# Kernel optimization log

Hardware: AMD Instinct MI355X
Metric: run time of the kernel (lower is better)

## Reference

```python
import jax, jax.numpy as jnp
import numpy as np

LAYER = 2
B, L, N, N2, S, M, D = 128, 50, 12, 12, 20, 12, 100


def _l2norm(x, eps=1e-12):
    # torch F.normalize: x / max(||x||_2, eps) over last dim
    n = jnp.sqrt(jnp.sum(x * x, axis=-1, keepdims=True))
    return x / jnp.maximum(n, eps)


def setup_inputs() -> dict:
    key = jax.random.key(0)
    ks = jax.random.split(key, 10)
    return {
        "sess_self": jax.random.normal(ks[0], (B, L, D), jnp.float32),
        "sess_neighbor": jax.random.normal(ks[1], (B, L, N, D), jnp.float32),
        "sess_neighbor2": jax.random.normal(ks[2], (B, L, N, N2, D), jnp.float32),
        "tar_self": jax.random.normal(ks[3], (B, S, D), jnp.float32),
        "tar_neighbor": jax.random.normal(ks[4], (B, S, M, D), jnp.float32),
        "w1": jax.random.normal(ks[5], (LAYER, D, D), jnp.float32) * 0.1,
        "w2": jax.random.normal(ks[6], (LAYER, D, 1), jnp.float32) * 0.1,
        "w3": jax.random.normal(ks[7], (LAYER, 2 * D, D), jnp.float32) * 0.1,
        "w4": jax.random.normal(ks[8], (LAYER, D, 1), jnp.float32) * 0.1,
        "session_len": jax.random.randint(ks[9], (B,), 1, 50).astype(jnp.int64),
    }


def _forward(sess_self, sess_neighbor, sess_neighbor2, tar_self, tar_neighbor, w1, w2, w3, w4):
    b, s = sess_self.shape[0], tar_self.shape[1]
    l, d = sess_self.shape[1], sess_self.shape[2]
    # sess_embedding_layer: list of [B,S,L,D]; target: list of [B,S,D]
    sess_layers = [jnp.broadcast_to(sess_self[:, None, :, :], (b, s, l, d))]
    tar_layers = [tar_self]
    sn = sess_neighbor  # may be updated by 2-hop aggregation
    for i in range(LAYER):
        # --- session neighbor attention: mul -> linear -> leaky_relu -> linear -> softmax(N) -> sum ---
        mean_sess = jnp.mean(sess_layers[i], axis=1)                     # [B,L,D]
        att = (mean_sess[:, :, None, :] * sn) @ w1[i]                    # [B,L,N,D]
        att = jax.nn.leaky_relu(att, negative_slope=0.2)
        att = jax.nn.softmax(att @ w2[i], axis=-2)                       # [B,L,N,1]
        total = jnp.sum(att * sn, axis=-2)                               # [B,L,D]
        emb = _l2norm(total)
        sess_layers.append(jnp.broadcast_to(emb[:, None, :, :], (b, s, l, d)))
        # --- 2-hop neighbor aggregation (only first layer when layer>1) ---
        if i <= 0 and LAYER > 1:
            att2 = (sn[:, :, :, None, :] * sess_neighbor2) @ w1[i]       # [B,L,N,N2,D]
            att2 = jax.nn.leaky_relu(att2, negative_slope=0.2)
            att2 = jax.nn.softmax(att2 @ w2[i], axis=-2)                 # [B,L,N,N2,1]
            sn = jnp.sum(att2 * sess_neighbor2, axis=-2)                 # [B,L,N,D]
        # --- target neighbor attention ---
        sess_last = sess_layers[i - 1][:, :, :1, :]                      # [B,S,1,D]
        t = tar_layers[i]                                                # [B,S,D]
        cat = jnp.concatenate(
            [t[:, :, None, :] * tar_neighbor, sess_last + tar_neighbor], axis=-1)  # [B,S,M,2D]
        a = jnp.tanh(cat @ w3[i])                                        # [B,S,M,D]
        a = jax.nn.softmax(a @ w4[i], axis=-2)                           # [B,S,M,1]
        tot = jnp.sum(a * tar_neighbor, axis=-2)                         # [B,S,D]
        ti = _l2norm((tot + tar_layers[0]) * 0.5)
        tar_layers.append(ti)
        tar_layers = tar_layers + tar_layers  # faithful: list doubles each layer
    return jnp.stack(sess_layers, axis=0), jnp.stack(tar_layers, axis=0)


def reference(sess_self, sess_neighbor, sess_neighbor2, tar_self, tar_neighbor, w1, w2, w3, w4, session_len):
    return _forward(sess_self, sess_neighbor, sess_neighbor2, tar_self, tar_neighbor, w1, w2, w3, w4)
```

## Files before the change

### kernel.cpp

```cpp
#include <hip/hip_runtime.h>
#include <cmath>

#define CB 128
#define CL 50
#define CN 12
#define CS 20
#define CM 12
#define CD 100

typedef __attribute__((ext_vector_type(8))) short short8;
typedef __attribute__((ext_vector_type(4))) float f32x4;

__device__ __forceinline__ unsigned short f2bf(float f) {
    unsigned int u = __float_as_uint(f);
    u += 0x7FFFu + ((u >> 16) & 1u);
    return (unsigned short)(u >> 16);
}
__device__ __forceinline__ float4 mul4(float4 a, float4 b) {
    return make_float4(a.x * b.x, a.y * b.y, a.z * b.z, a.w * b.w);
}
__device__ __forceinline__ float4 add4(float4 a, float4 b) {
    return make_float4(a.x + b.x, a.y + b.y, a.z + b.z, a.w + b.w);
}
__device__ __forceinline__ short8 pack8(float4 a, float4 b) {
    short8 v;
    v[0] = (short)f2bf(a.x); v[1] = (short)f2bf(a.y);
    v[2] = (short)f2bf(a.z); v[3] = (short)f2bf(a.w);
    v[4] = (short)f2bf(b.x); v[5] = (short)f2bf(b.y);
    v[6] = (short)f2bf(b.z); v[7] = (short)f2bf(b.w);
    return v;
}

__global__ void prep_weights_kernel(const float* __restrict__ w1,
                                    const float* __restrict__ w3,
                                    unsigned short* __restrict__ w1t,
                                    unsigned short* __restrict__ w3t)
{
    int idx = blockIdx.x * 256 + threadIdx.x;
    const int TOT1 = 2 * 112 * 128;
    const int TOT3 = 2 * 112 * 224;
    if (idx < TOT1) {
        int l = idx / (112 * 128);
        int r = idx - l * (112 * 128);
        int n = r / 128, k = r - (r / 128) * 128;
        float v = (n < CD && k < CD) ? w1[l * CD * CD + k * CD + n] : 0.f;
        w1t[idx] = f2bf(v);
    } else if (idx < TOT1 + TOT3) {
        int j = idx - TOT1;
        int l = j / (112 * 224);
        int r = j - l * (112 * 224);
        int n = r / 224, k = r - (r / 224) * 224;
        float v = (n < CD && k < 2 * CD) ? w3[l * 2 * CD * CD + k * CD + n] : 0.f;
        w3t[j] = f2bf(v);
    }
}

__global__ __launch_bounds__(256) void neigh_mfma_kernel(
    const float* __restrict__ a0, const float* __restrict__ c0,
    float* __restrict__ o0, int nb0, int l20,
    const float* __restrict__ a1, const float* __restrict__ c1,
    float* __restrict__ o1, int l21,
    const unsigned short* __restrict__ w1t,
    const float* __restrict__ w2)
{
    __shared__ __align__(16) unsigned short sB[112 * 128];

    const int tid = threadIdx.x;
    const int wave = tid >> 6, lane = tid & 63;
    const int lhi = lane >> 4, llo = lane & 15;

    const float *ap, *cp; float* op; int l2f, g0;
    if ((int)blockIdx.x < nb0) {
        ap = a0; cp = c0; op = o0; l2f = l20; g0 = blockIdx.x * 8;
    } else {
        ap = a1; cp = c1; op = o1; l2f = l21; g0 = (blockIdx.x - nb0) * 8;
    }

    for (int i = tid; i < 1792; i += 256) {
        int n = i >> 4, kc = i & 15;
        short8 v = *(const short8*)(w1t + n * 128 + kc * 8);
        char* dst = (char*)sB + n * 256 + ((kc ^ (n & 7)) << 4);
        *(short8*)dst = v;
    }

    short8 af[2][4];
#pragma unroll
    for (int mt = 0; mt < 2; ++mt) {
        const int g = g0 + wave * 2 + mt;
        const int n = (llo < CN) ? llo : 0;
        const float* cpr = cp + ((size_t)g * CN + n) * CD;
        const float* apr = ap + (size_t)g * CD;
#pragma unroll
        for (int ks = 0; ks < 4; ++ks) {
            const int k0 = ks * 32 + lhi * 8;
            if (ks < 3) {
                float4 cv0 = *(const float4*)(cpr + k0);
                float4 cv1 = *(const float4*)(cpr + k0 + 4);
                float4 av0 = *(const float4*)(apr + k0);
                float4 av1 = *(const float4*)(apr + k0 + 4);
                af[mt][ks] = pack8(mul4(av0, cv0), mul4(av1, cv1));
            } else if (lhi == 0) {
                float4 cv0 = *(const float4*)(cpr + 96);
                float4 av0 = *(const float4*)(apr + 96);
                float4 z = make_float4(0.f, 0.f, 0.f, 0.f);
                af[mt][ks] = pack8(mul4(av0, cv0), z);
            } else {
                af[mt][ks] = (short8){0, 0, 0, 0, 0, 0, 0, 0};
            }
        }
    }
    __syncthreads();

    f32x4 acc[2][7];
#pragma unroll
    for (int mt = 0; mt < 2; ++mt)
#pragma unroll
        for (int nt = 0; nt < 7; ++nt) acc[mt][nt] = (f32x4){0.f, 0.f, 0.f, 0.f};

    const char* pB = (const char*)sB;
    const int bxor = llo & 7;
#pragma unroll
    for (int ks = 0; ks < 4; ++ks) {
        const int kbq = ks * 4 + lhi;
#pragma unroll
        for (int nt = 0; nt < 7; ++nt) {
            short8 bfv = *(const short8*)(pB + (nt * 16 + llo) * 256 + ((kbq ^ bxor) << 4));
            acc[0][nt] = __builtin_amdgcn_mfma_f32_16x16x32_bf16(af[0][ks], bfv, acc[0][nt], 0, 0, 0);
            acc[1][nt] = __builtin_amdgcn_mfma_f32_16x16x32_bf16(af[1][ks], bfv, acc[1][nt], 0, 0, 0);
        }
    }

    float att[2][4];
#pragma unroll
    for (int mt = 0; mt < 2; ++mt) {
        float s[4] = {0.f, 0.f, 0.f, 0.f};
#pragma unroll
        for (int nt = 0; nt < 7; ++nt) {
            const int n = nt * 16 + llo;
            const float w2v = (n < CD) ? w2[n] : 0.f;
#pragma unroll
            for (int r = 0; r < 4; ++r) {
                float y = acc[mt][nt][r];
                y = (y >= 0.f) ? y : 0.2f * y;
                s[r] = fmaf(y, w2v, s[r]);
            }
        }
#pragma unroll
        for (int off = 1; off < 16; off <<= 1)
#pragma unroll
            for (int r = 0; r < 4; ++r) s[r] += __shfl_xor(s[r], off, 64);
        float pmax = -1e30f;
        if (lhi < 3) pmax = fmaxf(fmaxf(s[0], s[1]), fmaxf(s[2], s[3]));
        pmax = fmaxf(pmax, __shfl_xor(pmax, 16, 64));
        pmax = fmaxf(pmax, __shfl_xor(pmax, 32, 64));
        float e[4];
#pragma unroll
        for (int r = 0; r < 4; ++r) e[r] = (lhi < 3) ? __expf(s[r] - pmax) : 0.f;
        float ps = e[0] + e[1] + e[2] + e[3];
        ps += __shfl_xor(ps, 16, 64);
        ps += __shfl_xor(ps, 32, 64);
        const float inv = 1.f / ps;
#pragma unroll
        for (int r = 0; r < 4; ++r) att[mt][r] = e[r] * inv;
    }

    const bool act = lane < 50;
    const int d2 = lane * 2;
#pragma unroll
    for (int mt = 0; mt < 2; ++mt) {
        const int g = g0 + wave * 2 + mt;
        float2 tot = make_float2(0.f, 0.f);
        if (act) {
            const float* crow = cp + (size_t)g * CN * CD + d2;
#pragma unroll
            for (int n = 0; n < CN; ++n) {
                const float at = __shfl(att[mt][n & 3], (n >> 2) * 16, 64);
                float2 cv = *(const float2*)(crow + n * CD);
                tot.x = fmaf(at, cv.x, tot.x);
                tot.y = fmaf(at, cv.y, tot.y);
            }
        }
        if (l2f) {
            float sq = act ? (tot.x * tot.x + tot.y * tot.y) : 0.f;
#pragma unroll
            for (int off = 32; off > 0; off >>= 1) sq += __shfl_xor(sq, off, 64);
            const float rn = 1.f / fmaxf(sqrtf(sq), 1e-12f);
            tot.x *= rn; tot.y *= rn;
        }
        if (act) *(float2*)(op + (size_t)g * CD + d2) = tot;
    }
}

__device__ __forceinline__ int swzq28(int q, int x) {
    return q ^ ((q < 24) ? x : (x & 3));
}
__device__ __forceinline__ float4 xchunk(const float* __restrict__ tnr,
                                         const float* __restrict__ tv,
                                         const float* __restrict__ slv, int k) {
    if (k < CD)
        return mul4(*(const float4*)(tv + k), *(const float4*)(tnr + k));
    if (k < 2 * CD) {
        int k2 = k - CD;
        return add4(*(const float4*)(slv + k2), *(const float4*)(tnr + k2));
    }
    return make_float4(0.f, 0.f, 0.f, 0.f);
}

__global__ __launch_bounds__(256) void tar_mfma_kernel(
    const float* __restrict__ tvec,
    const float* __restrict__ sl,
    const float* __restrict__ tn,
    const unsigned short* __restrict__ w3t,
    const float* __restrict__ w4,
    const float* __restrict__ tar0,
    float* __restrict__ outp,
    int slStride)
{
    __shared__ __align__(16) unsigned short sB[112 * 224];

    const int tid = threadIdx.x;
    const int wave = tid >> 6, lane = tid & 63;
    const int lhi = lane >> 4, llo = lane & 15;
    const int g = blockIdx.x * 4 + wave;
    const int b = g / CS;

    for (int i = tid; i < 3136; i += 256) {
        int n = i / 28, kc = i - (i / 28) * 28;
        short8 v = *(const short8*)(w3t + n * 224 + kc * 8);
        char* dst = (char*)sB + n * 448 + (swzq28(kc, n & 7) << 4);
        *(short8*)dst = v;
    }

    short8 af[7];
    {
        const int m = (llo < CM) ? llo : 0;
        const float* tnr = tn + ((size_t)g * CM + m) * CD;
        const float* tv = tvec + (size_t)g * CD;
        const float* slv = sl + (size_t)b * slStride;
#pragma unroll
        for (int ks = 0; ks < 7; ++ks) {
            const int k0 = ks * 32 + lhi * 8;
            af[ks] = pack8(xchunk(tnr, tv, slv, k0),
                           xchunk(tnr, tv, slv, k0 + 4));
        }
    }
    __syncthreads();

    f32x4 acc[7];
#pragma unroll
    for (int nt = 0; nt < 7; ++nt) acc[nt] = (f32x4){0.f, 0.f, 0.f, 0.f};

    const char* pB = (const char*)sB;
    const int bxor = llo & 7;
#pragma unroll
    for (int ks = 0; ks < 7; ++ks) {
        const int kbq = ks * 4 + lhi;
#pragma unroll
        for (int nt = 0; nt < 7; ++nt) {
            short8 bfv = *(const short8*)(pB + (nt * 16 + llo) * 448 + (swzq28(kbq, bxor) << 4));
            acc[nt] = __builtin_amdgcn_mfma_f32_16x16x32_bf16(af[ks], bfv, acc[nt], 0, 0, 0);
        }
    }

    float s[4] = {0.f, 0.f, 0.f, 0.f};
#pragma unroll
    for (int nt = 0; nt < 7; ++nt) {
        const int n = nt * 16 + llo;
        const float w4v = (n < CD) ? w4[n] : 0.f;
#pragma unroll
        for (int r = 0; r < 4; ++r)
            s[r] = fmaf(tanhf(acc[nt][r]), w4v, s[r]);
    }
#pragma unroll
    for (int off = 1; off < 16; off <<= 1)
#pragma unroll
        for (int r = 0; r < 4; ++r) s[r] += __shfl_xor(s[r], off, 64);

    float pmax = -1e30f;
    if (lhi < 3) pmax = fmaxf(fmaxf(s[0], s[1]), fmaxf(s[2], s[3]));
    pmax = fmaxf(pmax, __shfl_xor(pmax, 16, 64));
    pmax = fmaxf(pmax, __shfl_xor(pmax, 32, 64));
    float e[4];
#pragma unroll
    for (int r = 0; r < 4; ++r) e[r] = (lhi < 3) ? __expf(s[r] - pmax) : 0.f;
    float ps = e[0] + e[1] + e[2] + e[3];
    ps += __shfl_xor(ps, 16, 64);
    ps += __shfl_xor(ps, 32, 64);
    const float inv = 1.f / ps;
    float att[4];
#pragma unroll
    for (int r = 0; r < 4; ++r) att[r] = e[r] * inv;

    const bool act = lane < 50;
    const int d2 = lane * 2;
    float2 tot = make_float2(0.f, 0.f);
    if (act) {
        const float* tnr = tn + (size_t)g * CM * CD + d2;
#pragma unroll
        for (int m = 0; m < CM; ++m) {
            const float at = __shfl(att[m & 3], (m >> 2) * 16, 64);
            float2 cv = *(const float2*)(tnr + m * CD);
            tot.x = fmaf(at, cv.x, tot.x);
            tot.y = fmaf(at, cv.y, tot.y);
        }
        float2 t0 = *(const float2*)(tar0 + (size_t)g * CD + d2);
        tot.x = (tot.x + t0.x) * 0.5f;
        tot.y = (tot.y + t0.y) * 0.5f;
    }
    float sq = act ? (tot.x * tot.x + tot.y * tot.y) : 0.f;
#pragma unroll
    for (int off = 32; off > 0; off >>= 1) sq += __shfl_xor(sq, off, 64);
    const float rn = 1.f / fmaxf(sqrtf(sq), 1e-12f);
    if (act) {
        tot.x *= rn; tot.y *= rn;
        *(float2*)(outp + (size_t)g * CD + d2) = tot;
    }
}

__global__ void assemble_kernel(
    const float* __restrict__ sess_self, const float* __restrict__ emb0,
    const float* __restrict__ emb1, const float* __restrict__ tar_self,
    const float* __restrict__ T1, const float* __restrict__ T2,
    f32x4* __restrict__ out)
{
    const int LD4 = CL * CD / 4;
    const int SLD4 = CS * LD4;
    const int LAY0 = CB * SLD4;
    const int TOT0 = 3 * LAY0;
    const int LAY1 = CB * CS * CD / 4;
    const int TOT = TOT0 + 10 * LAY1;

    for (int i = blockIdx.x * blockDim.x + threadIdx.x; i < TOT;
         i += gridDim.x * blockDim.x) {
        f32x4 v;
        if (i < TOT0) {
            int layer = i / LAY0;
            int r = i - layer * LAY0;
            int b = r / SLD4;
            int r2 = r - b * SLD4;
            int ld4 = r2 % LD4;
            const float* src = (layer == 0) ? sess_self : (layer == 1) ? emb0 : emb1;
            v = ((const f32x4*)src)[b * LD4 + ld4];
        } else {
            int j = i - TOT0;
            int layer = j / LAY1;
            int r = j - layer * LAY1;
            int k = layer % 5;
            const float* src = (k == 4) ? T2 : ((k == 1) || (k == 3)) ? T1 : tar_self;
            v = ((const f32x4*)src)[r];
        }
        __builtin_nontemporal_store(v, &out[i]);
    }
}

extern "C" void kernel_launch(void* const* d_in, const int* in_sizes, int n_in,
                              void* d_out, int out_size, void* d_ws, size_t ws_size,
                              hipStream_t stream)
{
    const float* sess_self      = (const float*)d_in[0];
    const float* sess_neighbor  = (const float*)d_in[1];
    const float* sess_neighbor2 = (const float*)d_in[2];
    const float* tar_self       = (const float*)d_in[3];
    const float* tar_neighbor   = (const float*)d_in[4];
    const float* w1             = (const float*)d_in[5];
    const float* w2             = (const float*)d_in[6];
    const float* w3             = (const float*)d_in[7];
    const float* w4             = (const float*)d_in[8];
    float* out = (float*)d_out;
    float* ws  = (float*)d_ws;

    float* emb0 = ws;
    float* emb1 = ws + 640000;
    float* sn1  = ws + 1280000;
    float* T1   = ws + 8960000;
    float* T2   = ws + 9216000;
    unsigned short* w1t = (unsigned short*)(ws + 9472000);
    unsigned short* w3t = w1t + 28672;

    prep_weights_kernel<<<308, 256, 0, stream>>>(w1, w3, w1t, w3t);

    neigh_mfma_kernel<<<10400, 256, 0, stream>>>(
        sess_self, sess_neighbor, emb0, 800, 1,
        sess_neighbor, sess_neighbor2, sn1, 0,
        w1t, w2);
    neigh_mfma_kernel<<<800, 256, 0, stream>>>(
        emb0, sn1, emb1, 800, 1,
        emb0, sn1, emb1, 1,
        w1t + 112 * 128, w2 + CD);
    tar_mfma_kernel<<<640, 256, 0, stream>>>(
        tar_self, emb0, tar_neighbor, w3t, w4, tar_self, T1, CL * CD);
    tar_mfma_kernel<<<640, 256, 0, stream>>>(
        T1, sess_self, tar_neighbor, w3t + 112 * 224, w4 + CD, tar_self, T2, CL * CD);

    assemble_kernel<<<2048, 256, 0, stream>>>(
        sess_self, emb0, emb1, tar_self, T1, T2, (f32x4*)out);
}
```

Measured before the change: 279.7 us.

## Stage neighbor rows into LDS via global_load_lds, read weights from global

Each wave copies its groups' neighbor and mean rows straight from global memory into LDS with async global_load_lds. The A-operand build and the weighted sum then both read from LDS, so the neighbor data is fetched from global once instead of twice. The shared W1 LDS tile and its block barrier are dropped, with B fragments read directly from global (L2-cached) memory, and w2 values are hoisted into registers. The cost is uncoalesced per-lane global reads of the B fragments inside the MFMA loop and possible LDS bank conflicts on the unswizzled row reads.

```diff
diff --git a/kernel.cpp b/kernel.cpp
--- a/kernel.cpp
+++ b/kernel.cpp
@@ -29,6 +29,13 @@
     v[4] = (short)f2bf(b.x); v[5] = (short)f2bf(b.y);
     v[6] = (short)f2bf(b.z); v[7] = (short)f2bf(b.w);
     return v;
+}
+
+__device__ __forceinline__ void gload_lds16(const float* gsrc, float* ldst) {
+    __builtin_amdgcn_global_load_lds(
+        (const __attribute__((address_space(1))) unsigned int*)gsrc,
+        (__attribute__((address_space(3))) unsigned int*)ldst,
+        16, 0, 0);
 }
 
 __global__ void prep_weights_kernel(const float* __restrict__ w1,
@@ -63,7 +70,8 @@
     const unsigned short* __restrict__ w1t,
     const float* __restrict__ w2)
 {
-    __shared__ __align__(16) unsigned short sB[112 * 128];
+    __shared__ __align__(16) float sC[8][1280];
+    __shared__ __align__(16) float sA[8][256];
 
     const int tid = threadIdx.x;
     const int wave = tid >> 6, lane = tid & 63;
@@ -76,32 +84,51 @@
         ap = a1; cp = c1; op = o1; l2f = l21; g0 = (blockIdx.x - nb0) * 8;
     }
 
-    for (int i = tid; i < 1792; i += 256) {
-        int n = i >> 4, kc = i & 15;
-        short8 v = *(const short8*)(w1t + n * 128 + kc * 8);
-        char* dst = (char*)sB + n * 256 + ((kc ^ (n & 7)) << 4);
-        *(short8*)dst = v;
-    }
+    float w2v[7];
+#pragma unroll
+    for (int nt = 0; nt < 7; ++nt) {
+        int n = nt * 16 + llo;
+        w2v[nt] = (n < CD) ? w2[n] : 0.f;
+    }
+
+#pragma unroll
+    for (int mt = 0; mt < 2; ++mt) {
+        const int gl = wave * 2 + mt;
+        const int g = g0 + gl;
+        const float* cbase = cp + (size_t)g * (CN * CD);
+        const float* abase = ap + (size_t)g * CD;
+#pragma unroll
+        for (int ch = 0; ch < 5; ++ch) {
+            int soff = ch * 256 + lane * 4;
+            if (soff > CN * CD - 4) soff = 0;
+            gload_lds16(cbase + soff, &sC[gl][ch * 256]);
+        }
+        int aoff = lane * 4;
+        if (aoff > CD - 4) aoff = 0;
+        gload_lds16(abase + aoff, &sA[gl][0]);
+    }
+    asm volatile("s_waitcnt vmcnt(0)" ::: "memory");
+    __builtin_amdgcn_sched_barrier(0);
 
     short8 af[2][4];
 #pragma unroll
     for (int mt = 0; mt < 2; ++mt) {
-        const int g = g0 + wave * 2 + mt;
+        const int gl = wave * 2 + mt;
         const int n = (llo < CN) ? llo : 0;
-        const float* cpr = cp + ((size_t)g * CN + n) * CD;
-        const float* apr = ap + (size_t)g * CD;
+        const float* crow = &sC[gl][n * CD];
+        const float* av = &sA[gl][0];
 #pragma unroll
         for (int ks = 0; ks < 4; ++ks) {
             const int k0 = ks * 32 + lhi * 8;
             if (ks < 3) {
-                float4 cv0 = *(const float4*)(cpr + k0);
-                float4 cv1 = *(const float4*)(cpr + k0 + 4);
-                float4 av0 = *(const float4*)(apr + k0);
-                float4 av1 = *(const float4*)(apr + k0 + 4);
+                float4 cv0 = *(const float4*)(crow + k0);
+                float4 cv1 = *(const float4*)(crow + k0 + 4);
+                float4 av0 = *(const float4*)(av + k0);
+                float4 av1 = *(const float4*)(av + k0 + 4);
                 af[mt][ks] = pack8(mul4(av0, cv0), mul4(av1, cv1));
             } else if (lhi == 0) {
-                float4 cv0 = *(const float4*)(cpr + 96);
-                float4 av0 = *(const float4*)(apr + 96);
+                float4 cv0 = *(const float4*)(crow + 96);
+                float4 av0 = *(const float4*)(av + 96);
                 float4 z = make_float4(0.f, 0.f, 0.f, 0.f);
                 af[mt][ks] = pack8(mul4(av0, cv0), z);
             } else {
@@ -109,7 +136,6 @@
             }
         }
     }
-    __syncthreads();
 
     f32x4 acc[2][7];
 #pragma unroll
@@ -117,14 +143,12 @@
 #pragma unroll
         for (int nt = 0; nt < 7; ++nt) acc[mt][nt] = (f32x4){0.f, 0.f, 0.f, 0.f};
 
-    const char* pB = (const char*)sB;
-    const int bxor = llo & 7;
 #pragma unroll
     for (int ks = 0; ks < 4; ++ks) {
         const int kbq = ks * 4 + lhi;
 #pragma unroll
         for (int nt = 0; nt < 7; ++nt) {
-            short8 bfv = *(const short8*)(pB + (nt * 16 + llo) * 256 + ((kbq ^ bxor) << 4));
+            short8 bfv = *(const short8*)(w1t + (nt * 16 + llo) * 128 + kbq * 8);
             acc[0][nt] = __builtin_amdgcn_mfma_f32_16x16x32_bf16(af[0][ks], bfv, acc[0][nt], 0, 0, 0);
             acc[1][nt] = __builtin_amdgcn_mfma_f32_16x16x32_bf16(af[1][ks], bfv, acc[1][nt], 0, 0, 0);
         }
@@ -136,13 +160,11 @@
         float s[4] = {0.f, 0.f, 0.f, 0.f};
 #pragma unroll
         for (int nt = 0; nt < 7; ++nt) {
-            const int n = nt * 16 + llo;
-            const float w2v = (n < CD) ? w2[n] : 0.f;
 #pragma unroll
             for (int r = 0; r < 4; ++r) {
                 float y = acc[mt][nt][r];
                 y = (y >= 0.f) ? y : 0.2f * y;
-                s[r] = fmaf(y, w2v, s[r]);
+                s[r] = fmaf(y, w2v[nt], s[r]);
             }
         }
 #pragma unroll
@@ -168,14 +190,14 @@
     const int d2 = lane * 2;
 #pragma unroll
     for (int mt = 0; mt < 2; ++mt) {
-        const int g = g0 + wave * 2 + mt;
+        const int gl = wave * 2 + mt;
+        const int g = g0 + gl;
         float2 tot = make_float2(0.f, 0.f);
         if (act) {
-            const float* crow = cp + (size_t)g * CN * CD + d2;
 #pragma unroll
             for (int n = 0; n < CN; ++n) {
                 const float at = __shfl(att[mt][n & 3], (n >> 2) * 16, 64);
-                float2 cv = *(const float2*)(crow + n * CD);
+                float2 cv = *(const float2*)(&sC[gl][n * CD + d2]);
                 tot.x = fmaf(at, cv.x, tot.x);
                 tot.y = fmaf(at, cv.y, tot.y);
             }
```

Result: slower. 332.3 us (+18.8%).
